# Optimization experiments

Measured on AMD Instinct MI355X. Metric: run time of the kernel, lower is better.

## Reference

```python
import jax, jax.numpy as jnp
import numpy as np

DIM = 1024
DEPTH = 4
VOCAB = 32000
B, N = 2, 2048
DFF = 4096
FG = 0.9  # frac_gradient_state_transition


def setup_inputs() -> dict:
    key = jax.random.key(0)
    ks = jax.random.split(key, 12)
    s = 0.02
    d = DIM
    return {
        "tokens": jax.random.randint(ks[0], (B, N), 0, VOCAB, dtype=jnp.int32),
        "emb": jax.random.normal(ks[1], (VOCAB, d), jnp.float32) * s,
        "g1": jnp.ones((DEPTH, d), jnp.float32),
        "Wqkv": jax.random.normal(ks[2], (DEPTH, d, 3 * d), jnp.float32) * s,
        "Wa": jax.random.normal(ks[3], (DEPTH, d, 2 * d), jnp.float32) * s,
        "ba": jnp.zeros((DEPTH, 2 * d), jnp.float32),
        "Wg": jax.random.normal(ks[4], (DEPTH, d, d), jnp.float32) * s,
        "Wo": jax.random.normal(ks[5], (DEPTH, d, d), jnp.float32) * s,
        "g2": jnp.ones((DEPTH, d), jnp.float32),
        "W1": jax.random.normal(ks[6], (DEPTH, d, DFF), jnp.float32) * s,
        "b1": jnp.zeros((DEPTH, DFF), jnp.float32),
        "W2": jax.random.normal(ks[7], (DEPTH, DFF, d), jnp.float32) * s,
        "b2": jnp.zeros((DEPTH, d), jnp.float32),
        "gf": jnp.ones((d,), jnp.float32),
        "Wl": jax.random.normal(ks[8], (d, VOCAB), jnp.float32) * s,
    }


def _rms(x, g):
    # F.normalize(x, dim=-1) * sqrt(dim) * gamma  (eps=1e-12 like torch)
    nrm = jnp.sqrt(jnp.sum(x * x, axis=-1, keepdims=True))
    return x / jnp.maximum(nrm, 1e-12) * (x.shape[-1] ** 0.5) * g


def _gate_loop(q, k, v, a):
    # q,k,v: (BH, n, 1) real; a: (BH, n, 1) complex
    kv = k[..., :, None] * v[..., None, :]          # (BH, n, 1, 1)
    a = a[..., None]                                 # (BH, n, 1, 1)
    a = jax.nn.sigmoid(jnp.abs(a)) * jnp.exp(1j * jnp.angle(a))  # polar(sigmoid(|a|), angle(a))

    def binop(c1, c2):
        a_i, kv_i = c1
        a_j, kv_j = c2
        return a_j * a_i, a_j.real * kv_i + kv_j

    _, kv = jax.lax.associative_scan(binop, (a, kv), axis=1)
    return jnp.einsum('bnd,bnde->bne', q, kv)        # (BH, n, 1)


def _attn(x, g1, Wqkv, Wa, ba, Wg, Wo):
    b, n, d = x.shape
    h = d  # heads == dim_inner, head dim == 1
    xn = _rms(x, g1)
    q, k, v = jnp.split(xn @ Wqkv, 3, axis=-1)       # each (b, n, d)
    split = lambda t: t.reshape(b, n, h, 1).transpose(0, 2, 1, 3).reshape(b * h, n, 1)
    q, k, v = split(q), split(k), split(v)
    al = (xn @ Wa + ba).reshape(b, n, h, 2).transpose(0, 2, 1, 3).reshape(b * h, n, 1, 2)
    a = al[..., 0] + 1j * al[..., 1]                 # (b*h, n, 1) complex
    a = FG * a + (1.0 - FG) * jax.lax.stop_gradient(a)
    out = _gate_loop(q, k, v, a)                     # (b*h, n, 1)
    out = out.reshape(b, h, n, 1).transpose(0, 2, 1, 3).reshape(b, n, d)
    gates = jax.nn.silu(xn @ Wg)
    return (gates * out) @ Wo


def _ff(x, g2, W1, b1, W2, b2):
    hdn = jax.nn.gelu(_rms(x, g2) @ W1 + b1, approximate=False)
    return hdn @ W2 + b2


def reference(tokens, emb, g1, Wqkv, Wa, ba, Wg, Wo, g2, W1, b1, W2, b2, gf, Wl):
    x = emb[tokens]                                  # (B, N, DIM)
    for i in range(DEPTH):
        x = x + _attn(x, g1[i], Wqkv[i], Wa[i], ba[i], Wg[i], Wo[i])
        x = x + _ff(x, g2[i], W1[i], b1[i], W2[i], b2[i])
    return _rms(x, gf) @ Wl                          # (B, N, VOCAB) logits
```

## Files before the change

### kernel.cpp

```cpp
#include <hip/hip_runtime.h>


typedef float fx4 __attribute__((ext_vector_type(4)));
typedef _Float16 f16x8 __attribute__((ext_vector_type(8)));
typedef _Float16 f16x4 __attribute__((ext_vector_type(4)));

#define AS1 __attribute__((address_space(1)))
#define AS3 __attribute__((address_space(3)))

__global__ __launch_bounds__(256) void transpose_f16_kernel(
    const float* __restrict__ in, _Float16* __restrict__ out,
    int K, int N, size_t ostride)
{
    __shared__ float tile[32][33];
    const int b = blockIdx.z;
    in  += (size_t)b * K * N;
    out += (size_t)b * ostride;
    const int k0 = blockIdx.x * 32, n0 = blockIdx.y * 32;
    const int tr = threadIdx.x >> 3;
    const int tc = (threadIdx.x & 7) * 4;
    fx4 v = *(const fx4*)&in[(size_t)(k0 + tr) * N + n0 + tc];
    tile[tr][tc + 0] = v[0]; tile[tr][tc + 1] = v[1];
    tile[tr][tc + 2] = v[2]; tile[tr][tc + 3] = v[3];
    __syncthreads();
    f16x4 o;
    #pragma unroll
    for (int e = 0; e < 4; ++e) o[e] = (_Float16)tile[tc + e][tr];
    *(f16x4*)&out[(size_t)(n0 + tr) * K + k0 + tc] = o;
}

__global__ __launch_bounds__(256) void embed_kernel(
    const int* __restrict__ tokens, const float* __restrict__ emb,
    float* __restrict__ x)
{
    const int row = blockIdx.x;
    const int t = tokens[row];
    const int c = threadIdx.x * 4;
    *(fx4*)&x[(size_t)row * 1024 + c] = *(const fx4*)&emb[(size_t)t * 1024 + c];
}

__global__ __launch_bounds__(256) void rms_f16_kernel(
    const float* __restrict__ x, const float* __restrict__ g,
    _Float16* __restrict__ outh)
{
    const int row = blockIdx.x;
    const int c = threadIdx.x * 4;
    fx4 v = *(const fx4*)&x[(size_t)row * 1024 + c];
    float ss = v[0]*v[0] + v[1]*v[1] + v[2]*v[2] + v[3]*v[3];
    #pragma unroll
    for (int off = 32; off > 0; off >>= 1) ss += __shfl_down(ss, off, 64);
    __shared__ float wsum[4];
    if ((threadIdx.x & 63) == 0) wsum[threadIdx.x >> 6] = ss;
    __syncthreads();
    const float nrm = sqrtf(wsum[0] + wsum[1] + wsum[2] + wsum[3]);
    const float scale = 32.0f / fmaxf(nrm, 1e-12f);
    fx4 gg = *(const fx4*)&g[c];
    f16x4 o;
    #pragma unroll
    for (int e = 0; e < 4; ++e) o[e] = (_Float16)(v[e] * scale * gg[e]);
    *(f16x4*)&outh[(size_t)row * 1024 + c] = o;
}

__global__ __launch_bounds__(256) void prep_qkv_kernel(
    const float* __restrict__ qkv, float* __restrict__ qT, float* __restrict__ kvT)
{
    __shared__ float tq[32][33], tkv[32][33];
    const int n0 = blockIdx.x * 32, h0 = blockIdx.y * 32, b = blockIdx.z;
    const int tr = threadIdx.x >> 3;
    const int tc = (threadIdx.x & 7) * 4;
    const float* row = qkv + ((size_t)b * 2048 + n0 + tr) * 3072;
    fx4 qv = *(const fx4*)&row[h0 + tc];
    fx4 kv = *(const fx4*)&row[1024 + h0 + tc];
    fx4 vv = *(const fx4*)&row[2048 + h0 + tc];
    #pragma unroll
    for (int e = 0; e < 4; ++e) { tq[tr][tc + e] = qv[e]; tkv[tr][tc + e] = kv[e] * vv[e]; }
    __syncthreads();
    fx4 oq, okv;
    #pragma unroll
    for (int e = 0; e < 4; ++e) { oq[e] = tq[tc + e][tr]; okv[e] = tkv[tc + e][tr]; }
    const size_t ob = ((size_t)b * 1024 + h0 + tr) * 2048 + n0 + tc;
    *(fx4*)&qT[ob] = oq;
    *(fx4*)&kvT[ob] = okv;
}

__global__ __launch_bounds__(256) void prep_a_kernel(
    const float* __restrict__ al, float* __restrict__ aReT, float* __restrict__ aImT)
{
    __shared__ float tre[32][33], tim[32][33];
    const int n0 = blockIdx.x * 32, h0 = blockIdx.y * 32, b = blockIdx.z;
    const int tr = threadIdx.x >> 3;
    const int tcf = (threadIdx.x & 7) * 8;
    const float* row = al + ((size_t)b * 2048 + n0 + tr) * 2048 + 2 * h0;
    fx4 v0 = *(const fx4*)&row[tcf];
    fx4 v1 = *(const fx4*)&row[tcf + 4];
    #pragma unroll
    for (int p = 0; p < 4; ++p) {
        float re = (p < 2) ? v0[2 * p] : v1[2 * (p - 2)];
        float im = (p < 2) ? v0[2 * p + 1] : v1[2 * (p - 2) + 1];
        float r = sqrtf(re * re + im * im);
        float sg = 1.0f / (1.0f + expf(-r));
        float a_re, a_im;
        if (r > 0.0f) { float inv = sg / r; a_re = re * inv; a_im = im * inv; }
        else          { a_re = sg; a_im = 0.0f; }
        tre[tr][tcf / 2 + p] = a_re;
        tim[tr][tcf / 2 + p] = a_im;
    }
    __syncthreads();
    const int tc = (threadIdx.x & 7) * 4;
    fx4 ore, oim;
    #pragma unroll
    for (int e = 0; e < 4; ++e) { ore[e] = tre[tc + e][tr]; oim[e] = tim[tc + e][tr]; }
    const size_t ob = ((size_t)b * 1024 + h0 + tr) * 2048 + n0 + tc;
    *(fx4*)&aReT[ob] = ore;
    *(fx4*)&aImT[ob] = oim;
}

__device__ __forceinline__ int pidx(int i) { return i + (i >> 5); }

__global__ __launch_bounds__(256) void scanT_kernel(
    const float* __restrict__ kvT, const float* __restrict__ aReT,
    const float* __restrict__ aImT, const float* __restrict__ qT,
    float* __restrict__ yT)
{
    const int tid = threadIdx.x;
    const size_t base = (size_t)blockIdx.x * 2048;
    __shared__ float s_re[2048 + 64], s_im[2048 + 64], s_kv[2048 + 64];

    for (int i = tid; i < 512; i += 256) {
        fx4 kv = *(const fx4*)&kvT[base + i * 4];
        fx4 re = *(const fx4*)&aReT[base + i * 4];
        fx4 im = *(const fx4*)&aImT[base + i * 4];
        #pragma unroll
        for (int e = 0; e < 4; ++e) {
            const int j = pidx(i * 4 + e);
            s_kv[j] = kv[e]; s_re[j] = re[e]; s_im[j] = im[e];
        }
    }
    __syncthreads();

    for (int d = 0; d < 11; ++d) {
        const int half = 1 << d, stride = half << 1;
        const int npairs = 2048 >> (d + 1);
        for (int i = tid; i < npairs; i += 256) {
            const int rj = pidx(i * stride + stride - 1);
            const int lj = pidx(i * stride + stride - 1 - half);
            float lre = s_re[lj], lim = s_im[lj], lkv = s_kv[lj];
            float rre = s_re[rj], rim = s_im[rj], rkv = s_kv[rj];
            s_kv[rj] = rre * lkv + rkv;
            s_re[rj] = rre * lre - rim * lim;
            s_im[rj] = rre * lim + rim * lre;
        }
        __syncthreads();
    }
    for (int d = 9; d >= 0; --d) {
        const int w = 1 << d;
        const int nupd = (2048 >> (d + 1)) - 1;
        for (int t = tid; t < nupd; t += 256) {
            const int i = t + 1;
            const int rj = pidx((2 * i + 1) * w - 1);
            const int lj = pidx(2 * i * w - 1);
            float lre = s_re[lj], lim = s_im[lj], lkv = s_kv[lj];
            float rre = s_re[rj], rim = s_im[rj], rkv = s_kv[rj];
            s_kv[rj] = rre * lkv + rkv;
            s_re[rj] = rre * lre - rim * lim;
            s_im[rj] = rre * lim + rim * lre;
        }
        __syncthreads();
    }
    for (int i = tid; i < 512; i += 256) {
        fx4 q = *(const fx4*)&qT[base + i * 4];
        fx4 o;
        #pragma unroll
        for (int e = 0; e < 4; ++e) o[e] = q[e] * s_kv[pidx(i * 4 + e)];
        *(fx4*)&yT[base + i * 4] = o;
    }
}

__global__ __launch_bounds__(256) void gate_kernel(
    const float* __restrict__ G, const float* __restrict__ yT,
    _Float16* __restrict__ gated)
{
    __shared__ float ty[32][33];
    const int n0 = blockIdx.x * 32, h0 = blockIdx.y * 32, b = blockIdx.z;
    const int tr = threadIdx.x >> 3;
    const int tc = (threadIdx.x & 7) * 4;
    fx4 yv = *(const fx4*)&yT[((size_t)b * 1024 + h0 + tr) * 2048 + n0 + tc];
    #pragma unroll
    for (int e = 0; e < 4; ++e) ty[tr][tc + e] = yv[e];
    __syncthreads();
    const size_t grow = ((size_t)b * 2048 + n0 + tr) * 1024 + h0 + tc;
    fx4 gv = *(const fx4*)&G[grow];
    f16x4 o;
    #pragma unroll
    for (int e = 0; e < 4; ++e) {
        const float s = gv[e] / (1.0f + expf(-gv[e]));
        o[e] = (_Float16)(s * ty[tc + e][tr]);
    }
    *(f16x4*)&gated[grow] = o;
}

template<int EPI>
__global__ __launch_bounds__(512) void gemm_kernel(
    const _Float16* __restrict__ A, const _Float16* __restrict__ Bt,
    const float* __restrict__ bias,
    float* __restrict__ Cf, float* __restrict__ Cf2, float* __restrict__ Cf3,
    _Float16* __restrict__ Ch,
    int M, int N, int K)
{
    __shared__ __align__(16) _Float16 As[256 * 64];
    __shared__ __align__(16) _Float16 Bs[128 * 64];
    const int tid  = threadIdx.x;
    const int lane = tid & 63;
    const int wave = tid >> 6;
    const int bm = blockIdx.x, bn = blockIdx.y;
    const int wm = (wave >> 1) * 64;
    const int wn = (wave & 1) * 64;

    fx4 acc[4][4] = {};

    const size_t aRow0 = (size_t)bm * 256;
    const size_t bRow0 = (size_t)bn * 128;

    for (int k0 = 0; k0 < K; k0 += 64) {
        #pragma unroll
        for (int q = 0; q < 4; ++q) {
            const int chunk = q * 512 + tid;
            const int row = chunk >> 3;
            const int slot = chunk & 7;
            const int gs = slot ^ (row & 7);
            const size_t aoff = (aRow0 + row) * K + k0 + gs * 8;
            __builtin_amdgcn_global_load_lds((const AS1 void*)(A + aoff),
                (AS3 void*)((char*)As + chunk * 16), 16, 0, 0);
        }
        #pragma unroll
        for (int q = 0; q < 2; ++q) {
            const int chunk = q * 512 + tid;
            const int row = chunk >> 3;
            const int slot = chunk & 7;
            const int gs = slot ^ (row & 7);
            const size_t boff = (bRow0 + row) * K + k0 + gs * 8;
            __builtin_amdgcn_global_load_lds((const AS1 void*)(Bt + boff),
                (AS3 void*)((char*)Bs + chunk * 16), 16, 0, 0);
        }
        __syncthreads();

        #pragma unroll
        for (int kk = 0; kk < 2; ++kk) {
            const int sw = ((kk * 4 + (lane >> 4)) ^ (lane & 7)) * 16;
            f16x8 af[4], bf[4];
            #pragma unroll
            for (int i = 0; i < 4; ++i) {
                const int row = wm + i * 16 + (lane & 15);
                af[i] = *(const f16x8*)((const char*)As + row * 128 + sw);
            }
            #pragma unroll
            for (int j = 0; j < 4; ++j) {
                const int row = wn + j * 16 + (lane & 15);
                bf[j] = *(const f16x8*)((const char*)Bs + row * 128 + sw);
            }
            #pragma unroll
            for (int i = 0; i < 4; ++i)
                #pragma unroll
                for (int j = 0; j < 4; ++j)
                    acc[i][j] = __builtin_amdgcn_mfma_f32_16x16x32_f16(
                        af[i], bf[j], acc[i][j], 0, 0, 0);
        }
        __syncthreads();
    }

    const int col_l = lane & 15, row_l = (lane >> 4) * 4;
    #pragma unroll
    for (int i = 0; i < 4; ++i) {
        #pragma unroll
        for (int j = 0; j < 4; ++j) {
            #pragma unroll
            for (int r = 0; r < 4; ++r) {
                const int row = bm * 256 + wm + i * 16 + row_l + r;
                const int col = bn * 128 + wn + j * 16 + col_l;
                const float v = acc[i][j][r];
                if (EPI == 0) {
                    Cf[(size_t)row * N + col] = v;
                } else if (EPI == 2) {
                    Cf[(size_t)row * N + col] += v;
                } else if (EPI == 3) {
                    Cf[(size_t)row * N + col] += v + bias[col];
                } else if (EPI == 4) {
                    const float t = v + bias[col];
                    const float gelu = 0.5f * t * (1.0f + erff(t * 0.70710678118654752f));
                    Ch[(size_t)row * N + col] = (_Float16)gelu;
                } else if (EPI == 6) {
                    if (bn < 24)      Cf [(size_t)row * 3072 + col] = v;
                    else if (bn < 40) Cf2[(size_t)row * 2048 + (col - 3072)] = v + bias[col - 3072];
                    else              Cf3[(size_t)row * 1024 + (col - 5120)] = v;
                }
            }
        }
    }
}

extern "C" void kernel_launch(void* const* d_in, const int* in_sizes, int n_in,
                              void* d_out, int out_size, void* d_ws, size_t ws_size,
                              hipStream_t stream)
{
    const int*   tokens = (const int*)d_in[0];
    const float* emb  = (const float*)d_in[1];
    const float* g1   = (const float*)d_in[2];
    const float* Wqkv = (const float*)d_in[3];
    const float* Wa   = (const float*)d_in[4];
    const float* ba   = (const float*)d_in[5];
    const float* Wg   = (const float*)d_in[6];
    const float* Wo   = (const float*)d_in[7];
    const float* g2   = (const float*)d_in[8];
    const float* W1   = (const float*)d_in[9];
    const float* b1   = (const float*)d_in[10];
    const float* W2   = (const float*)d_in[11];
    const float* b2   = (const float*)d_in[12];
    const float* gf   = (const float*)d_in[13];
    const float* Wl   = (const float*)d_in[14];
    float* out = (float*)d_out;

    char* ws = (char*)d_ws;
    size_t off = 0;
    auto take = [&](size_t bytes) {
        char* p = ws + off; off += (bytes + 255) & ~(size_t)255; return p;
    };

    _Float16* wcat = (_Float16*)take((size_t)4 * 6144 * 1024 * 2);
    _Float16* wo   = (_Float16*)take((size_t)4 * 1024 * 1024 * 2);
    _Float16* w1   = (_Float16*)take((size_t)4 * 4096 * 1024 * 2);
    _Float16* w2   = (_Float16*)take((size_t)4 * 1024 * 4096 * 2);
    char*     wlRegion = take((size_t)64 << 20);
    _Float16* wl   = (_Float16*)wlRegion;
    float*    x    = (float*)take((size_t)4096 * 1024 * 4);
    _Float16* xn   = (_Float16*)take((size_t)4096 * 1024 * 2);
    float*    qkvb = (float*)take((size_t)4096 * 3072 * 4);
    float*    alb  = (float*)take((size_t)4096 * 2048 * 4);
    float*    G    = (float*)take((size_t)4096 * 1024 * 4);

    float* qT   = (float*)wlRegion;
    float* kvT  = (float*)(wlRegion + ((size_t)16 << 20));
    float* aReT = (float*)(wlRegion + ((size_t)32 << 20));
    float* aImT = (float*)(wlRegion + ((size_t)48 << 20));
    float*    yT    = alb;
    _Float16* gated = (_Float16*)((char*)alb + ((size_t)16 << 20));
    _Float16* h     = (_Float16*)qkvb;

    const dim3 blk(256);
    const dim3 gblk(512);

    transpose_f16_kernel<<<dim3(32,  96, 4), blk, 0, stream>>>(Wqkv, wcat,               1024, 3072, (size_t)6144 * 1024);
    transpose_f16_kernel<<<dim3(32,  64, 4), blk, 0, stream>>>(Wa,   wcat + 3072 * 1024, 1024, 2048, (size_t)6144 * 1024);
    transpose_f16_kernel<<<dim3(32,  32, 4), blk, 0, stream>>>(Wg,   wcat + 5120 * 1024, 1024, 1024, (size_t)6144 * 1024);
    transpose_f16_kernel<<<dim3(32,  32, 4), blk, 0, stream>>>(Wo,   wo,  1024, 1024, (size_t)1024 * 1024);
    transpose_f16_kernel<<<dim3(32, 128, 4), blk, 0, stream>>>(W1,   w1,  1024, 4096, (size_t)4096 * 1024);
    transpose_f16_kernel<<<dim3(128, 32, 4), blk, 0, stream>>>(W2,   w2,  4096, 1024, (size_t)1024 * 4096);

    embed_kernel<<<4096, blk, 0, stream>>>(tokens, emb, x);

    for (int i = 0; i < 4; ++i) {
        rms_f16_kernel<<<4096, blk, 0, stream>>>(x, g1 + i * 1024, xn);
        gemm_kernel<6><<<dim3(16, 48), gblk, 0, stream>>>(
            xn, wcat + (size_t)i * 6144 * 1024, ba + i * 2048,
            qkvb, alb, G, nullptr, 4096, 6144, 1024);
        prep_qkv_kernel<<<dim3(64, 32, 2), blk, 0, stream>>>(qkvb, qT, kvT);
        prep_a_kernel<<<dim3(64, 32, 2), blk, 0, stream>>>(alb, aReT, aImT);
        scanT_kernel<<<2048, blk, 0, stream>>>(kvT, aReT, aImT, qT, yT);
        gate_kernel<<<dim3(64, 32, 2), blk, 0, stream>>>(G, yT, gated);
        gemm_kernel<2><<<dim3(16, 8), gblk, 0, stream>>>(
            gated, wo + (size_t)i * 1024 * 1024, nullptr,
            x, nullptr, nullptr, nullptr, 4096, 1024, 1024);
        rms_f16_kernel<<<4096, blk, 0, stream>>>(x, g2 + i * 1024, xn);
        gemm_kernel<4><<<dim3(16, 32), gblk, 0, stream>>>(
            xn, w1 + (size_t)i * 4096 * 1024, b1 + i * 4096,
            nullptr, nullptr, nullptr, h, 4096, 4096, 1024);
        gemm_kernel<3><<<dim3(16, 8), gblk, 0, stream>>>(
            h, w2 + (size_t)i * 1024 * 4096, b2 + i * 1024,
            x, nullptr, nullptr, nullptr, 4096, 1024, 4096);
    }

    transpose_f16_kernel<<<dim3(32, 1000, 1), blk, 0, stream>>>(Wl, wl, 1024, 32000, 0);

    rms_f16_kernel<<<4096, blk, 0, stream>>>(x, gf, xn);
    gemm_kernel<0><<<dim3(16, 250), gblk, 0, stream>>>(
        xn, wl, nullptr, out, nullptr, nullptr, nullptr, 4096, 32000, 1024);
}
```

Measured before the change: 1.838 ms.

## Templatize GEMM tile sizes, split-K the W2 GEMM, retile Wo and logits GEMMs

The GEMM kernel takes BM/BN as template parameters and gets a separate leading dimension so it can run split-K over blockIdx.z. The FF down-projection (K=4096) is split into two K halves that write partial sums, and a new combine kernel adds them plus the bias into the residual. The Wo GEMM moves to 128x128 tiles so it launches more blocks, and the final logits GEMM uses 256x256 tiles with 1024 threads. The aim is better CU occupancy on the small-grid GEMMs, at the cost of extra partial-sum traffic, an extra launch, and more register and LDS pressure on the large tile.

```diff
diff --git a/kernel.cpp b/kernel.cpp
--- a/kernel.cpp
+++ b/kernel.cpp
@@ -199,46 +199,70 @@
     *(f16x4*)&gated[grow] = o;
 }
 
-template<int EPI>
-__global__ __launch_bounds__(512) void gemm_kernel(
+__global__ __launch_bounds__(256) void combine2_kernel(
+    const float* __restrict__ p, const float* __restrict__ bias,
+    float* __restrict__ x)
+{
+    const size_t i = ((size_t)blockIdx.x * 256 + threadIdx.x) * 4;
+    fx4 a = *(const fx4*)&p[i];
+    fx4 b = *(const fx4*)&p[i + (size_t)4096 * 1024];
+    fx4 xx = *(const fx4*)&x[i];
+    fx4 bb = *(const fx4*)&bias[(int)(i & 1023)];
+    fx4 o;
+    #pragma unroll
+    for (int e = 0; e < 4; ++e) o[e] = xx[e] + (a[e] + b[e] + bb[e]);
+    *(fx4*)&x[i] = o;
+}
+
+template<int EPI, int BM, int BN>
+__global__ __launch_bounds__(BM * BN / 64) void gemm_kernel(
     const _Float16* __restrict__ A, const _Float16* __restrict__ Bt,
     const float* __restrict__ bias,
     float* __restrict__ Cf, float* __restrict__ Cf2, float* __restrict__ Cf3,
     _Float16* __restrict__ Ch,
-    int M, int N, int K)
-{
-    __shared__ __align__(16) _Float16 As[256 * 64];
-    __shared__ __align__(16) _Float16 Bs[128 * 64];
+    int M, int N, int K, int Kld)
+{
+    constexpr int THREADS = BM * BN / 64;
+    constexpr int NW = BN / 64;
+    __shared__ __align__(16) _Float16 As[BM * 64];
+    __shared__ __align__(16) _Float16 Bs[BN * 64];
     const int tid  = threadIdx.x;
     const int lane = tid & 63;
     const int wave = tid >> 6;
     const int bm = blockIdx.x, bn = blockIdx.y;
-    const int wm = (wave >> 1) * 64;
-    const int wn = (wave & 1) * 64;
+    const int bz = blockIdx.z;
+    const int wm = (wave / NW) * 64;
+    const int wn = (wave % NW) * 64;
+
+    A  += (size_t)bz * K;
+    Bt += (size_t)bz * K;
+    if (EPI == 0) Cf += (size_t)bz * M * N;
 
     fx4 acc[4][4] = {};
 
-    const size_t aRow0 = (size_t)bm * 256;
-    const size_t bRow0 = (size_t)bn * 128;
+    const size_t aRow0 = (size_t)bm * BM;
+    const size_t bRow0 = (size_t)bn * BN;
 
     for (int k0 = 0; k0 < K; k0 += 64) {
-        #pragma unroll
-        for (int q = 0; q < 4; ++q) {
-            const int chunk = q * 512 + tid;
+        constexpr int QA = BM * 8 / THREADS;
+        #pragma unroll
+        for (int q = 0; q < QA; ++q) {
+            const int chunk = q * THREADS + tid;
             const int row = chunk >> 3;
             const int slot = chunk & 7;
             const int gs = slot ^ (row & 7);
-            const size_t aoff = (aRow0 + row) * K + k0 + gs * 8;
+            const size_t aoff = (aRow0 + row) * (size_t)Kld + k0 + gs * 8;
             __builtin_amdgcn_global_load_lds((const AS1 void*)(A + aoff),
                 (AS3 void*)((char*)As + chunk * 16), 16, 0, 0);
         }
-        #pragma unroll
-        for (int q = 0; q < 2; ++q) {
-            const int chunk = q * 512 + tid;
+        constexpr int QB = BN * 8 / THREADS;
+        #pragma unroll
+        for (int q = 0; q < QB; ++q) {
+            const int chunk = q * THREADS + tid;
             const int row = chunk >> 3;
             const int slot = chunk & 7;
             const int gs = slot ^ (row & 7);
-            const size_t boff = (bRow0 + row) * K + k0 + gs * 8;
+            const size_t boff = (bRow0 + row) * (size_t)Kld + k0 + gs * 8;
             __builtin_amdgcn_global_load_lds((const AS1 void*)(Bt + boff),
                 (AS3 void*)((char*)Bs + chunk * 16), 16, 0, 0);
         }
@@ -275,15 +299,13 @@
         for (int j = 0; j < 4; ++j) {
             #pragma unroll
             for (int r = 0; r < 4; ++r) {
-                const int row = bm * 256 + wm + i * 16 + row_l + r;
-                const int col = bn * 128 + wn + j * 16 + col_l;
+                const int row = bm * BM + wm + i * 16 + row_l + r;
+                const int col = bn * BN + wn + j * 16 + col_l;
                 const float v = acc[i][j][r];
                 if (EPI == 0) {
                     Cf[(size_t)row * N + col] = v;
                 } else if (EPI == 2) {
                     Cf[(size_t)row * N + col] += v;
-                } else if (EPI == 3) {
-                    Cf[(size_t)row * N + col] += v + bias[col];
                 } else if (EPI == 4) {
                     const float t = v + bias[col];
                     const float gelu = 0.5f * t * (1.0f + erff(t * 0.70710678118654752f));
@@ -344,9 +366,9 @@
     float*    yT    = alb;
     _Float16* gated = (_Float16*)((char*)alb + ((size_t)16 << 20));
     _Float16* h     = (_Float16*)qkvb;
+    float*    part  = alb;
 
     const dim3 blk(256);
-    const dim3 gblk(512);
 
     transpose_f16_kernel<<<dim3(32,  96, 4), blk, 0, stream>>>(Wqkv, wcat,               1024, 3072, (size_t)6144 * 1024);
     transpose_f16_kernel<<<dim3(32,  64, 4), blk, 0, stream>>>(Wa,   wcat + 3072 * 1024, 1024, 2048, (size_t)6144 * 1024);
@@ -359,28 +381,29 @@
 
     for (int i = 0; i < 4; ++i) {
         rms_f16_kernel<<<4096, blk, 0, stream>>>(x, g1 + i * 1024, xn);
-        gemm_kernel<6><<<dim3(16, 48), gblk, 0, stream>>>(
+        gemm_kernel<6, 256, 128><<<dim3(16, 48), dim3(512), 0, stream>>>(
             xn, wcat + (size_t)i * 6144 * 1024, ba + i * 2048,
-            qkvb, alb, G, nullptr, 4096, 6144, 1024);
+            qkvb, alb, G, nullptr, 4096, 6144, 1024, 1024);
         prep_qkv_kernel<<<dim3(64, 32, 2), blk, 0, stream>>>(qkvb, qT, kvT);
         prep_a_kernel<<<dim3(64, 32, 2), blk, 0, stream>>>(alb, aReT, aImT);
         scanT_kernel<<<2048, blk, 0, stream>>>(kvT, aReT, aImT, qT, yT);
         gate_kernel<<<dim3(64, 32, 2), blk, 0, stream>>>(G, yT, gated);
-        gemm_kernel<2><<<dim3(16, 8), gblk, 0, stream>>>(
+        gemm_kernel<2, 128, 128><<<dim3(32, 8), blk, 0, stream>>>(
             gated, wo + (size_t)i * 1024 * 1024, nullptr,
-            x, nullptr, nullptr, nullptr, 4096, 1024, 1024);
+            x, nullptr, nullptr, nullptr, 4096, 1024, 1024, 1024);
         rms_f16_kernel<<<4096, blk, 0, stream>>>(x, g2 + i * 1024, xn);
-        gemm_kernel<4><<<dim3(16, 32), gblk, 0, stream>>>(
+        gemm_kernel<4, 256, 128><<<dim3(16, 32), dim3(512), 0, stream>>>(
             xn, w1 + (size_t)i * 4096 * 1024, b1 + i * 4096,
-            nullptr, nullptr, nullptr, h, 4096, 4096, 1024);
-        gemm_kernel<3><<<dim3(16, 8), gblk, 0, stream>>>(
-            h, w2 + (size_t)i * 1024 * 4096, b2 + i * 1024,
-            x, nullptr, nullptr, nullptr, 4096, 1024, 4096);
+            nullptr, nullptr, nullptr, h, 4096, 4096, 1024, 1024);
+        gemm_kernel<0, 256, 128><<<dim3(16, 8, 2), dim3(512), 0, stream>>>(
+            h, w2 + (size_t)i * 1024 * 4096, nullptr,
+            part, nullptr, nullptr, nullptr, 4096, 1024, 2048, 4096);
+        combine2_kernel<<<4096, blk, 0, stream>>>(part, b2 + i * 1024, x);
     }
 
     transpose_f16_kernel<<<dim3(32, 1000, 1), blk, 0, stream>>>(Wl, wl, 1024, 32000, 0);
 
     rms_f16_kernel<<<4096, blk, 0, stream>>>(x, gf, xn);
-    gemm_kernel<0><<<dim3(16, 250), gblk, 0, stream>>>(
-        xn, wl, nullptr, out, nullptr, nullptr, nullptr, 4096, 32000, 1024);
-}
+    gemm_kernel<0, 256, 256><<<dim3(16, 125), dim3(1024), 0, stream>>>(
+        xn, wl, nullptr, out, nullptr, nullptr, nullptr, 4096, 32000, 1024, 1024);
+}
```

Result: faster. 1.713 ms (-6.8%).
